# Performance work log

Measured on AMD Instinct MI355X. Metric: run time of the kernel, lower is better.

Reference implementation:

```python
import jax, jax.numpy as jnp
import numpy as np

B, S, D_IN, D_OUT, H = 2, 2048, 1024, 1024, 16
HEAD = D_OUT // H

def setup_inputs() -> dict:
    key = jax.random.key(0)
    ks = jax.random.split(key, 5)
    scale = 0.02
    return {
        "x": jax.random.normal(ks[0], (B, S, D_IN), dtype=jnp.float32),
        "Wq": jax.random.normal(ks[1], (D_OUT, D_IN), dtype=jnp.float32) * scale,
        "Wk": jax.random.normal(ks[2], (D_OUT, D_IN), dtype=jnp.float32) * scale,
        "Wv": jax.random.normal(ks[3], (D_OUT, D_IN), dtype=jnp.float32) * scale,
        "Wo": jax.random.normal(ks[4], (D_OUT, D_OUT), dtype=jnp.float32) * scale,
        "bo": jnp.zeros((D_OUT,), dtype=jnp.float32),
    }

def reference(x, Wq, Wk, Wv, Wo, bo):
    b, n, _ = x.shape
    # linear projections (torch Linear: y = x @ W.T)
    q = (x @ Wq.T).reshape(b, n, H, HEAD).transpose(0, 2, 1, 3)  # [b,h,n,d]
    k = (x @ Wk.T).reshape(b, n, H, HEAD).transpose(0, 2, 1, 3)
    v = (x @ Wv.T).reshape(b, n, H, HEAD).transpose(0, 2, 1, 3)
    scores = jnp.einsum('bhqd,bhkd->bhqk', q, k)  # [b,h,n,n]
    causal = jnp.triu(jnp.ones((n, n), dtype=bool), k=1)
    scores = jnp.where(causal, -jnp.inf, scores)
    # NOTE: original scales by sqrt(d_out**0.5) == d_out**0.25 (faithful quirk)
    inv_scale = jnp.float32(1.0 / (D_OUT ** 0.25))
    attn = jax.nn.softmax(scores * inv_scale, axis=-1)
    ctx = jnp.einsum('bhqk,bhkd->bhqd', attn, v)  # [b,h,n,d]
    ctx = ctx.transpose(0, 2, 1, 3).reshape(b, n, D_OUT)
    return ctx @ Wo.T + bo
```

## Files before the change

### kernel.cpp

```cpp
#include <hip/hip_runtime.h>

#define NB 2
#define NH 16
#define SEQ 2048
#define DM 1024
#define HD 64
#define MT (NB * SEQ)

typedef __attribute__((ext_vector_type(8))) short bf16x8;
typedef __attribute__((ext_vector_type(4))) float f32x4;

__device__ __forceinline__ unsigned short f2bf(float f) {
  union { float f; unsigned u; } v; v.f = f;
  return (unsigned short)((v.u + 0x7fffu + ((v.u >> 16) & 1u)) >> 16);
}

__device__ __forceinline__ void gld_lds16(const unsigned short* g, unsigned short* l) {
  __builtin_amdgcn_global_load_lds((const __attribute__((address_space(1))) unsigned int*)g,
                                   (__attribute__((address_space(3))) unsigned int*)l, 16, 0, 0);
}

__global__ __launch_bounds__(256) void cvt_all(const float* __restrict__ x,
                                               const float* __restrict__ wq,
                                               const float* __restrict__ wk,
                                               const float* __restrict__ wv,
                                               const float* __restrict__ wo,
                                               unsigned short* __restrict__ dst) {
  const int XQ = (MT * DM) / 4;
  const int WQ = (DM * DM) / 4;
  int i = blockIdx.x * 256 + threadIdx.x;
  const float* src; int base;
  if (i < XQ)               { src = x;  base = 0; }
  else if (i < XQ + WQ)     { src = wq; base = XQ; }
  else if (i < XQ + 2 * WQ) { src = wk; base = XQ + WQ; }
  else if (i < XQ + 3 * WQ) { src = wv; base = XQ + 2 * WQ; }
  else                      { src = wo; base = XQ + 3 * WQ; }
  float4 f = ((const float4*)src)[i - base];
  ushort4 u;
  u.x = f2bf(f.x); u.y = f2bf(f.y); u.z = f2bf(f.z); u.w = f2bf(f.w);
  ((ushort4*)dst)[i] = u;
}

#define LDT 32

__device__ __forceinline__ void gemm_bt_mainloop(const unsigned short* __restrict__ A,
                                                 const unsigned short* __restrict__ B,
                                                 int K,
                                                 unsigned short* As, unsigned short* Bs,
                                                 f32x4 acc[4][4]) {
  int tid = threadIdx.x;
  int lane = tid & 63, l15 = lane & 15, quad = lane >> 4;
  int w = tid >> 6, wm = (w >> 1) * 64, wn = (w & 1) * 64;
  int c0 = tid, c1 = tid + 256;
  int r0 = c0 >> 2, cc0 = (c0 & 3) * 8;
  int r1 = c1 >> 2, cc1 = (c1 & 3) * 8;
  const unsigned short* a0 = A + (size_t)r0 * K + cc0;
  const unsigned short* a1 = A + (size_t)r1 * K + cc1;
  const unsigned short* b0 = B + (size_t)r0 * K + cc0;
  const unsigned short* b1 = B + (size_t)r1 * K + cc1;
  unsigned short* la0 = As + c0 * 8;
  unsigned short* la1 = As + c1 * 8;
  unsigned short* lb0 = Bs + c0 * 8;
  unsigned short* lb1 = Bs + c1 * 8;

  for (int k0 = 0; k0 < K; k0 += 32) {
    gld_lds16(a0 + k0, la0);
    gld_lds16(a1 + k0, la1);
    gld_lds16(b0 + k0, lb0);
    gld_lds16(b1 + k0, lb1);
    __syncthreads();
    bf16x8 a[4], b[4];
#pragma unroll
    for (int i = 0; i < 4; ++i)
      a[i] = *(const bf16x8*)(As + (wm + i * 16 + l15) * LDT + 8 * quad);
#pragma unroll
    for (int i = 0; i < 4; ++i)
      b[i] = *(const bf16x8*)(Bs + (wn + i * 16 + l15) * LDT + 8 * quad);
#pragma unroll
    for (int i = 0; i < 4; ++i)
#pragma unroll
      for (int jj = 0; jj < 4; ++jj)
        acc[i][jj] = __builtin_amdgcn_mfma_f32_16x16x32_bf16(a[i], b[jj], acc[i][jj], 0, 0, 0);
    __syncthreads();
  }
}

#define QSCALE 0.2550565444f

__global__ __launch_bounds__(256) void gemm_qkv(const unsigned short* __restrict__ xb,
                                                const unsigned short* __restrict__ wcat,
                                                unsigned short* __restrict__ qb,
                                                unsigned short* __restrict__ kb,
                                                unsigned short* __restrict__ vtb) {
  __shared__ unsigned short As[128 * LDT], Bs[128 * LDT];
  int m0 = blockIdx.y * 128, n0 = blockIdx.x * 128;
  f32x4 acc[4][4];
#pragma unroll
  for (int i = 0; i < 4; ++i)
#pragma unroll
    for (int j = 0; j < 4; ++j) acc[i][j] = (f32x4){0.f, 0.f, 0.f, 0.f};

  gemm_bt_mainloop(xb + (size_t)m0 * DM, wcat + (size_t)n0 * DM, DM, As, Bs, acc);

  int tid = threadIdx.x, lane = tid & 63, l15 = lane & 15, quad = lane >> 4;
  int w = tid >> 6, wm = (w >> 1) * 64, wn = (w & 1) * 64;
  int mat = n0 >> 10;
#pragma unroll
  for (int i = 0; i < 4; ++i) {
    int mbase = m0 + wm + i * 16 + quad * 4;
    int bi = mbase >> 11, s = mbase & 2047;
#pragma unroll
    for (int j = 0; j < 4; ++j) {
      int n = n0 + wn + j * 16 + l15;
      int c = n & 1023, h = c >> 6, d = c & 63;
      if (mat == 2) {
        ushort4 u;
        u.x = f2bf(acc[i][j][0]); u.y = f2bf(acc[i][j][1]);
        u.z = f2bf(acc[i][j][2]); u.w = f2bf(acc[i][j][3]);
        *(ushort4*)(vtb + ((size_t)((bi * NH + h) * HD + d)) * SEQ + s) = u;
      } else {
        unsigned short* dst = (mat == 0) ? qb : kb;
        float sc = (mat == 0) ? QSCALE : 1.0f;
#pragma unroll
        for (int reg = 0; reg < 4; ++reg)
          dst[((size_t)((bi * NH + h) * SEQ + (s + reg))) * HD + d] = f2bf(acc[i][j][reg] * sc);
      }
    }
  }
}

#define LDQ 72

__global__ __launch_bounds__(512, 4) void attn_kernel(const unsigned short* __restrict__ qb,
                                                      const unsigned short* __restrict__ kb,
                                                      const unsigned short* __restrict__ vtb,
                                                      unsigned short* __restrict__ ctx) {
  __shared__ unsigned short QPs[128 * LDQ];
  __shared__ unsigned short Ks[64 * LDQ], Vts[64 * LDQ];
  int bx = blockIdx.x, h = blockIdx.y, bi = blockIdx.z;
  int qst = bi ? (15 - bx) : bx;
  int q0 = qst * 128;
  int tid = threadIdx.x, lane = tid & 63, l15 = lane & 15, quad = lane >> 4, w = tid >> 6;

  const unsigned short* qbase = qb + ((size_t)(bi * NH + h) * SEQ + q0) * HD;
  const unsigned short* kbase = kb + ((size_t)(bi * NH + h) * SEQ) * HD;
  const unsigned short* vbase = vtb + ((size_t)(bi * NH + h) * HD) * SEQ;

  {
    int c = tid, r = c >> 3, cc = (c & 7) * 8;
    *(int4*)(QPs + r * LDQ + cc) = *(const int4*)(qbase + (size_t)r * HD + cc);
    c = tid + 512; r = c >> 3; cc = (c & 7) * 8;
    *(int4*)(QPs + r * LDQ + cc) = *(const int4*)(qbase + (size_t)r * HD + cc);
  }
  int sr = tid >> 3, sc = (tid & 7) * 8;
  const unsigned short* kS = kbase + (size_t)sr * HD + sc;
  const unsigned short* vS = vbase + (size_t)sr * SEQ + sc;
  int4 kreg = *(const int4*)kS;
  int4 vreg = *(const int4*)vS;
  unsigned short* Kdst = Ks + sr * LDQ + sc;
  unsigned short* Vdst = Vts + sr * LDQ + sc;
  __syncthreads();

  bf16x8 aq0 = *(const bf16x8*)(QPs + (w * 16 + l15) * LDQ + 8 * quad);
  bf16x8 aq1 = *(const bf16x8*)(QPs + (w * 16 + l15) * LDQ + 32 + 8 * quad);

  f32x4 Oacc[4];
#pragma unroll
  for (int i = 0; i < 4; ++i) Oacc[i] = (f32x4){0.f, 0.f, 0.f, 0.f};
  float l_i[4] = {0.f, 0.f, 0.f, 0.f};
  int q0w = q0 + w * 16;
  int nkv = 2 * qst + 2;

  for (int j = 0; j < nkv; ++j) {
    int kv0 = j * 64;
    __syncthreads();
    *(int4*)Kdst = kreg;
    *(int4*)Vdst = vreg;
    __syncthreads();
    if (j + 1 < nkv) {
      kreg = *(const int4*)(kS + (size_t)(j + 1) * 64 * HD);
      vreg = *(const int4*)(vS + (j + 1) * 64);
    }
    if (kv0 <= q0w + 15) {
      f32x4 sacc[4];
#pragma unroll
      for (int ns = 0; ns < 4; ++ns) {
        bf16x8 bk0 = *(const bf16x8*)(Ks + (ns * 16 + l15) * LDQ + 8 * quad);
        bf16x8 bk1 = *(const bf16x8*)(Ks + (ns * 16 + l15) * LDQ + 32 + 8 * quad);
        sacc[ns] = (f32x4){0.f, 0.f, 0.f, 0.f};
        sacc[ns] = __builtin_amdgcn_mfma_f32_16x16x32_bf16(aq0, bk0, sacc[ns], 0, 0, 0);
        sacc[ns] = __builtin_amdgcn_mfma_f32_16x16x32_bf16(aq1, bk1, sacc[ns], 0, 0, 0);
      }
      bool needmask = (kv0 + 63) > q0w;
      float rs[4] = {0.f, 0.f, 0.f, 0.f};
#pragma unroll
      for (int ns = 0; ns < 4; ++ns)
#pragma unroll
        for (int reg = 0; reg < 4; ++reg) {
          float xv = sacc[ns][reg];
          if (needmask) {
            int kvg = kv0 + ns * 16 + l15;
            int qg = q0w + quad * 4 + reg;
            if (kvg > qg) xv = -INFINITY;
          }
          float p = __builtin_amdgcn_exp2f(xv);
          rs[reg] += p;
          QPs[(w * 16 + quad * 4 + reg) * LDQ + ns * 16 + l15] = f2bf(p);
        }
#pragma unroll
      for (int off = 1; off < 16; off <<= 1)
#pragma unroll
        for (int reg = 0; reg < 4; ++reg)
          rs[reg] += __shfl_xor(rs[reg], off, 64);
#pragma unroll
      for (int reg = 0; reg < 4; ++reg) l_i[reg] += rs[reg];

      bf16x8 pa0 = *(const bf16x8*)(QPs + (w * 16 + l15) * LDQ + 8 * quad);
      bf16x8 pa1 = *(const bf16x8*)(QPs + (w * 16 + l15) * LDQ + 32 + 8 * quad);
#pragma unroll
      for (int nd = 0; nd < 4; ++nd) {
        bf16x8 bv0 = *(const bf16x8*)(Vts + (nd * 16 + l15) * LDQ + 8 * quad);
        bf16x8 bv1 = *(const bf16x8*)(Vts + (nd * 16 + l15) * LDQ + 32 + 8 * quad);
        Oacc[nd] = __builtin_amdgcn_mfma_f32_16x16x32_bf16(pa0, bv0, Oacc[nd], 0, 0, 0);
        Oacc[nd] = __builtin_amdgcn_mfma_f32_16x16x32_bf16(pa1, bv1, Oacc[nd], 0, 0, 0);
      }
    }
  }

  float rl[4];
#pragma unroll
  for (int reg = 0; reg < 4; ++reg) rl[reg] = 1.0f / l_i[reg];
#pragma unroll
  for (int nd = 0; nd < 4; ++nd)
#pragma unroll
    for (int reg = 0; reg < 4; ++reg) {
      int s = q0w + quad * 4 + reg;
      int col = h * HD + nd * 16 + l15;
      ctx[((size_t)(bi * SEQ + s)) * DM + col] = f2bf(Oacc[nd][reg] * rl[reg]);
    }
}

__global__ __launch_bounds__(256) void gemm_out(const unsigned short* __restrict__ ctx,
                                                const unsigned short* __restrict__ wob,
                                                const float* __restrict__ bo,
                                                float* __restrict__ out) {
  __shared__ unsigned short As[128 * LDT], Bs[128 * LDT];
  int m0 = blockIdx.y * 128, n0 = blockIdx.x * 128;
  f32x4 acc[4][4];
#pragma unroll
  for (int i = 0; i < 4; ++i)
#pragma unroll
    for (int j = 0; j < 4; ++j) acc[i][j] = (f32x4){0.f, 0.f, 0.f, 0.f};

  gemm_bt_mainloop(ctx + (size_t)m0 * DM, wob + (size_t)n0 * DM, DM, As, Bs, acc);

  int tid = threadIdx.x, lane = tid & 63, l15 = lane & 15, quad = lane >> 4;
  int w = tid >> 6, wm = (w >> 1) * 64, wn = (w & 1) * 64;
#pragma unroll
  for (int i = 0; i < 4; ++i)
#pragma unroll
    for (int j = 0; j < 4; ++j) {
      int n = n0 + wn + j * 16 + l15;
      float bias = bo[n];
#pragma unroll
      for (int reg = 0; reg < 4; ++reg) {
        int m = m0 + wm + i * 16 + quad * 4 + reg;
        out[(size_t)m * DM + n] = acc[i][j][reg] + bias;
      }
    }
}

extern "C" void kernel_launch(void* const* d_in, const int* in_sizes, int n_in,
                              void* d_out, int out_size, void* d_ws, size_t ws_size,
                              hipStream_t stream) {
  const float* x  = (const float*)d_in[0];
  const float* Wq = (const float*)d_in[1];
  const float* Wk = (const float*)d_in[2];
  const float* Wv = (const float*)d_in[3];
  const float* Wo = (const float*)d_in[4];
  const float* bo = (const float*)d_in[5];
  float* out = (float*)d_out;

  unsigned short* ws = (unsigned short*)d_ws;
  unsigned short* xb   = ws;
  unsigned short* ctx  = ws;
  unsigned short* wcat = ws + (size_t)MT * DM;
  unsigned short* wob  = wcat + (size_t)3 * DM * DM;
  unsigned short* qb   = wob + (size_t)DM * DM;
  unsigned short* kb   = qb + (size_t)MT * DM;
  unsigned short* vtb  = kb + (size_t)MT * DM;

  int totalq = (MT * DM + 4 * DM * DM) / 4;
  cvt_all<<<totalq / 256, 256, 0, stream>>>(x, Wq, Wk, Wv, Wo, ws);

  gemm_qkv<<<dim3(24, 32), 256, 0, stream>>>(xb, wcat, qb, kb, vtb);
  attn_kernel<<<dim3(16, NH, NB), 512, 0, stream>>>(qb, kb, vtb, ctx);
  gemm_out<<<dim3(8, 32), 256, 0, stream>>>(ctx, wob, bo, out);
}
```

Measured before the change: 208.4 us.

## Widen GEMM K-tile with XOR-swizzled LDS and use 128-wide KV tiles in attention

The shared GEMM mainloop now stages 64-wide K slices with an XOR swizzle on the LDS layout, which halves the number of barrier pairs and is meant to avoid bank conflicts. Both GEMMs also get a launch-bounds occupancy hint. The attention kernel processes 128-key tiles per iteration and skips score MFMAs past the causal diagonal on the last tile, zero-filling the leftover P columns. It also converts P to bf16 by truncation instead of round-to-nearest, trading a small amount of precision for fewer ALU ops. LDS use and register pressure per block grow.

```diff
diff --git a/kernel.cpp b/kernel.cpp
--- a/kernel.cpp
+++ b/kernel.cpp
@@ -41,8 +41,6 @@
   ((ushort4*)dst)[i] = u;
 }
 
-#define LDT 32
-
 __device__ __forceinline__ void gemm_bt_mainloop(const unsigned short* __restrict__ A,
                                                  const unsigned short* __restrict__ B,
                                                  int K,
@@ -51,48 +49,55 @@
   int tid = threadIdx.x;
   int lane = tid & 63, l15 = lane & 15, quad = lane >> 4;
   int w = tid >> 6, wm = (w >> 1) * 64, wn = (w & 1) * 64;
-  int c0 = tid, c1 = tid + 256;
-  int r0 = c0 >> 2, cc0 = (c0 & 3) * 8;
-  int r1 = c1 >> 2, cc1 = (c1 & 3) * 8;
-  const unsigned short* a0 = A + (size_t)r0 * K + cc0;
-  const unsigned short* a1 = A + (size_t)r1 * K + cc1;
-  const unsigned short* b0 = B + (size_t)r0 * K + cc0;
-  const unsigned short* b1 = B + (size_t)r1 * K + cc1;
-  unsigned short* la0 = As + c0 * 8;
-  unsigned short* la1 = As + c1 * 8;
-  unsigned short* lb0 = Bs + c0 * 8;
-  unsigned short* lb1 = Bs + c1 * 8;
-
-  for (int k0 = 0; k0 < K; k0 += 32) {
-    gld_lds16(a0 + k0, la0);
-    gld_lds16(a1 + k0, la1);
-    gld_lds16(b0 + k0, lb0);
-    gld_lds16(b1 + k0, lb1);
+  int gofs[4];
+#pragma unroll
+  for (int it = 0; it < 4; ++it) {
+    int c = tid + it * 256;
+    int r = c >> 3, pos = c & 7;
+    gofs[it] = r * K + ((pos ^ (r & 7)) * 8);
+  }
+  for (int k0 = 0; k0 < K; k0 += 64) {
+#pragma unroll
+    for (int it = 0; it < 4; ++it)
+      gld_lds16(A + k0 + gofs[it], As + (tid + it * 256) * 8);
+#pragma unroll
+    for (int it = 0; it < 4; ++it)
+      gld_lds16(B + k0 + gofs[it], Bs + (tid + it * 256) * 8);
     __syncthreads();
-    bf16x8 a[4], b[4];
-#pragma unroll
-    for (int i = 0; i < 4; ++i)
-      a[i] = *(const bf16x8*)(As + (wm + i * 16 + l15) * LDT + 8 * quad);
-#pragma unroll
-    for (int i = 0; i < 4; ++i)
-      b[i] = *(const bf16x8*)(Bs + (wn + i * 16 + l15) * LDT + 8 * quad);
-#pragma unroll
-    for (int i = 0; i < 4; ++i)
-#pragma unroll
-      for (int jj = 0; jj < 4; ++jj)
-        acc[i][jj] = __builtin_amdgcn_mfma_f32_16x16x32_bf16(a[i], b[jj], acc[i][jj], 0, 0, 0);
+    bf16x8 a[4][2], b[4][2];
+#pragma unroll
+    for (int i = 0; i < 4; ++i) {
+      int row = wm + i * 16 + l15, sw = row & 7;
+#pragma unroll
+      for (int s = 0; s < 2; ++s)
+        a[i][s] = *(const bf16x8*)(As + row * 64 + (((quad + 4 * s) ^ sw) * 8));
+    }
+#pragma unroll
+    for (int i = 0; i < 4; ++i) {
+      int row = wn + i * 16 + l15, sw = row & 7;
+#pragma unroll
+      for (int s = 0; s < 2; ++s)
+        b[i][s] = *(const bf16x8*)(Bs + row * 64 + (((quad + 4 * s) ^ sw) * 8));
+    }
+#pragma unroll
+    for (int s = 0; s < 2; ++s)
+#pragma unroll
+      for (int i = 0; i < 4; ++i)
+#pragma unroll
+        for (int jj = 0; jj < 4; ++jj)
+          acc[i][jj] = __builtin_amdgcn_mfma_f32_16x16x32_bf16(a[i][s], b[jj][s], acc[i][jj], 0, 0, 0);
     __syncthreads();
   }
 }
 
 #define QSCALE 0.2550565444f
 
-__global__ __launch_bounds__(256) void gemm_qkv(const unsigned short* __restrict__ xb,
-                                                const unsigned short* __restrict__ wcat,
-                                                unsigned short* __restrict__ qb,
-                                                unsigned short* __restrict__ kb,
-                                                unsigned short* __restrict__ vtb) {
-  __shared__ unsigned short As[128 * LDT], Bs[128 * LDT];
+__global__ __launch_bounds__(256, 3) void gemm_qkv(const unsigned short* __restrict__ xb,
+                                                   const unsigned short* __restrict__ wcat,
+                                                   unsigned short* __restrict__ qb,
+                                                   unsigned short* __restrict__ kb,
+                                                   unsigned short* __restrict__ vtb) {
+  __shared__ unsigned short As[128 * 64], Bs[128 * 64];
   int m0 = blockIdx.y * 128, n0 = blockIdx.x * 128;
   f32x4 acc[4][4];
 #pragma unroll
@@ -129,14 +134,17 @@
   }
 }
 
-#define LDQ 72
+#define LP 136
+#define LDK 72
+#define LV 136
 
 __global__ __launch_bounds__(512, 4) void attn_kernel(const unsigned short* __restrict__ qb,
                                                       const unsigned short* __restrict__ kb,
                                                       const unsigned short* __restrict__ vtb,
                                                       unsigned short* __restrict__ ctx) {
-  __shared__ unsigned short QPs[128 * LDQ];
-  __shared__ unsigned short Ks[64 * LDQ], Vts[64 * LDQ];
+  __shared__ unsigned short Ps[128 * LP];
+  __shared__ unsigned short Ks[128 * LDK];
+  __shared__ unsigned short Vts[64 * LV];
   int bx = blockIdx.x, h = blockIdx.y, bi = blockIdx.z;
   int qst = bi ? (15 - bx) : bx;
   int q0 = qst * 128;
@@ -148,81 +156,99 @@
 
   {
     int c = tid, r = c >> 3, cc = (c & 7) * 8;
-    *(int4*)(QPs + r * LDQ + cc) = *(const int4*)(qbase + (size_t)r * HD + cc);
+    *(int4*)(Ps + r * LP + cc) = *(const int4*)(qbase + (size_t)r * HD + cc);
     c = tid + 512; r = c >> 3; cc = (c & 7) * 8;
-    *(int4*)(QPs + r * LDQ + cc) = *(const int4*)(qbase + (size_t)r * HD + cc);
-  }
-  int sr = tid >> 3, sc = (tid & 7) * 8;
-  const unsigned short* kS = kbase + (size_t)sr * HD + sc;
-  const unsigned short* vS = vbase + (size_t)sr * SEQ + sc;
-  int4 kreg = *(const int4*)kS;
-  int4 vreg = *(const int4*)vS;
-  unsigned short* Kdst = Ks + sr * LDQ + sc;
-  unsigned short* Vdst = Vts + sr * LDQ + sc;
+    *(int4*)(Ps + r * LP + cc) = *(const int4*)(qbase + (size_t)r * HD + cc);
+  }
+  int kr = tid >> 3, kc = (tid & 7) * 8;
+  int vr = tid >> 4, vc = (tid & 15) * 8;
+  const unsigned short* kS0 = kbase + (size_t)kr * HD + kc;
+  const unsigned short* kS1 = kS0 + (size_t)64 * HD;
+  const unsigned short* vS0 = vbase + (size_t)vr * SEQ + vc;
+  const unsigned short* vS1 = vS0 + (size_t)32 * SEQ;
+  int4 kreg0 = *(const int4*)kS0, kreg1 = *(const int4*)kS1;
+  int4 vreg0 = *(const int4*)vS0, vreg1 = *(const int4*)vS1;
+  unsigned short* Kd0 = Ks + kr * LDK + kc;
+  unsigned short* Kd1 = Kd0 + 64 * LDK;
+  unsigned short* Vd0 = Vts + vr * LV + vc;
+  unsigned short* Vd1 = Vd0 + 32 * LV;
   __syncthreads();
 
-  bf16x8 aq0 = *(const bf16x8*)(QPs + (w * 16 + l15) * LDQ + 8 * quad);
-  bf16x8 aq1 = *(const bf16x8*)(QPs + (w * 16 + l15) * LDQ + 32 + 8 * quad);
+  bf16x8 aq0 = *(const bf16x8*)(Ps + (w * 16 + l15) * LP + 8 * quad);
+  bf16x8 aq1 = *(const bf16x8*)(Ps + (w * 16 + l15) * LP + 32 + 8 * quad);
 
   f32x4 Oacc[4];
 #pragma unroll
   for (int i = 0; i < 4; ++i) Oacc[i] = (f32x4){0.f, 0.f, 0.f, 0.f};
   float l_i[4] = {0.f, 0.f, 0.f, 0.f};
   int q0w = q0 + w * 16;
-  int nkv = 2 * qst + 2;
-
-  for (int j = 0; j < nkv; ++j) {
-    int kv0 = j * 64;
+  int nt = qst + 1;
+
+  for (int j = 0; j < nt; ++j) {
+    int kv0 = j * 128;
     __syncthreads();
-    *(int4*)Kdst = kreg;
-    *(int4*)Vdst = vreg;
+    *(int4*)Kd0 = kreg0; *(int4*)Kd1 = kreg1;
+    *(int4*)Vd0 = vreg0; *(int4*)Vd1 = vreg1;
     __syncthreads();
-    if (j + 1 < nkv) {
-      kreg = *(const int4*)(kS + (size_t)(j + 1) * 64 * HD);
-      vreg = *(const int4*)(vS + (j + 1) * 64);
-    }
-    if (kv0 <= q0w + 15) {
-      f32x4 sacc[4];
-#pragma unroll
-      for (int ns = 0; ns < 4; ++ns) {
-        bf16x8 bk0 = *(const bf16x8*)(Ks + (ns * 16 + l15) * LDQ + 8 * quad);
-        bf16x8 bk1 = *(const bf16x8*)(Ks + (ns * 16 + l15) * LDQ + 32 + 8 * quad);
-        sacc[ns] = (f32x4){0.f, 0.f, 0.f, 0.f};
-        sacc[ns] = __builtin_amdgcn_mfma_f32_16x16x32_bf16(aq0, bk0, sacc[ns], 0, 0, 0);
-        sacc[ns] = __builtin_amdgcn_mfma_f32_16x16x32_bf16(aq1, bk1, sacc[ns], 0, 0, 0);
-      }
-      bool needmask = (kv0 + 63) > q0w;
-      float rs[4] = {0.f, 0.f, 0.f, 0.f};
-#pragma unroll
-      for (int ns = 0; ns < 4; ++ns)
-#pragma unroll
-        for (int reg = 0; reg < 4; ++reg) {
-          float xv = sacc[ns][reg];
-          if (needmask) {
-            int kvg = kv0 + ns * 16 + l15;
-            int qg = q0w + quad * 4 + reg;
-            if (kvg > qg) xv = -INFINITY;
-          }
-          float p = __builtin_amdgcn_exp2f(xv);
-          rs[reg] += p;
-          QPs[(w * 16 + quad * 4 + reg) * LDQ + ns * 16 + l15] = f2bf(p);
+    if (j + 1 < nt) {
+      size_t ko = (size_t)(j + 1) * 128 * HD;
+      int vo = (j + 1) * 128;
+      kreg0 = *(const int4*)(kS0 + ko); kreg1 = *(const int4*)(kS1 + ko);
+      vreg0 = *(const int4*)(vS0 + vo); vreg1 = *(const int4*)(vS1 + vo);
+    }
+    bool diag = (j == nt - 1);
+    int ns_hi = diag ? ((q0w + 15 - kv0) >> 4) : 7;
+    int s_hi = ns_hi >> 1;
+
+    float rs[4] = {0.f, 0.f, 0.f, 0.f};
+#pragma unroll
+    for (int ns = 0; ns < 8; ++ns) {
+      if (ns > ns_hi) break;
+      bf16x8 bk0 = *(const bf16x8*)(Ks + (ns * 16 + l15) * LDK + 8 * quad);
+      bf16x8 bk1 = *(const bf16x8*)(Ks + (ns * 16 + l15) * LDK + 32 + 8 * quad);
+      f32x4 s = (f32x4){0.f, 0.f, 0.f, 0.f};
+      s = __builtin_amdgcn_mfma_f32_16x16x32_bf16(aq0, bk0, s, 0, 0, 0);
+      s = __builtin_amdgcn_mfma_f32_16x16x32_bf16(aq1, bk1, s, 0, 0, 0);
+      bool m = diag && (ns == ns_hi);
+#pragma unroll
+      for (int reg = 0; reg < 4; ++reg) {
+        float xv = s[reg];
+        if (m) {
+          int kvg = kv0 + ns * 16 + l15;
+          int qg = q0w + quad * 4 + reg;
+          if (kvg > qg) xv = -INFINITY;
         }
-#pragma unroll
-      for (int off = 1; off < 16; off <<= 1)
+        float p = __builtin_amdgcn_exp2f(xv);
+        rs[reg] += p;
+        union { float f; unsigned u; } pu; pu.f = p;
+        Ps[(w * 16 + quad * 4 + reg) * LP + ns * 16 + l15] = (unsigned short)(pu.u >> 16);
+      }
+    }
+    if (diag) {
+#pragma unroll
+      for (int ns = 0; ns < 8; ++ns) {
+        if (ns <= ns_hi || ns > 2 * s_hi + 1) continue;
 #pragma unroll
         for (int reg = 0; reg < 4; ++reg)
-          rs[reg] += __shfl_xor(rs[reg], off, 64);
-#pragma unroll
-      for (int reg = 0; reg < 4; ++reg) l_i[reg] += rs[reg];
-
-      bf16x8 pa0 = *(const bf16x8*)(QPs + (w * 16 + l15) * LDQ + 8 * quad);
-      bf16x8 pa1 = *(const bf16x8*)(QPs + (w * 16 + l15) * LDQ + 32 + 8 * quad);
+          Ps[(w * 16 + quad * 4 + reg) * LP + ns * 16 + l15] = 0;
+      }
+    }
+#pragma unroll
+    for (int off = 1; off < 16; off <<= 1)
+#pragma unroll
+      for (int reg = 0; reg < 4; ++reg)
+        rs[reg] += __shfl_xor(rs[reg], off, 64);
+#pragma unroll
+    for (int reg = 0; reg < 4; ++reg) l_i[reg] += rs[reg];
+
+#pragma unroll
+    for (int step = 0; step < 4; ++step) {
+      if (step > s_hi) break;
+      bf16x8 pa = *(const bf16x8*)(Ps + (w * 16 + l15) * LP + 8 * quad + 32 * step);
 #pragma unroll
       for (int nd = 0; nd < 4; ++nd) {
-        bf16x8 bv0 = *(const bf16x8*)(Vts + (nd * 16 + l15) * LDQ + 8 * quad);
-        bf16x8 bv1 = *(const bf16x8*)(Vts + (nd * 16 + l15) * LDQ + 32 + 8 * quad);
-        Oacc[nd] = __builtin_amdgcn_mfma_f32_16x16x32_bf16(pa0, bv0, Oacc[nd], 0, 0, 0);
-        Oacc[nd] = __builtin_amdgcn_mfma_f32_16x16x32_bf16(pa1, bv1, Oacc[nd], 0, 0, 0);
+        bf16x8 bv = *(const bf16x8*)(Vts + (nd * 16 + l15) * LV + 8 * quad + 32 * step);
+        Oacc[nd] = __builtin_amdgcn_mfma_f32_16x16x32_bf16(pa, bv, Oacc[nd], 0, 0, 0);
       }
     }
   }
@@ -240,11 +266,11 @@
     }
 }
 
-__global__ __launch_bounds__(256) void gemm_out(const unsigned short* __restrict__ ctx,
-                                                const unsigned short* __restrict__ wob,
-                                                const float* __restrict__ bo,
-                                                float* __restrict__ out) {
-  __shared__ unsigned short As[128 * LDT], Bs[128 * LDT];
+__global__ __launch_bounds__(256, 3) void gemm_out(const unsigned short* __restrict__ ctx,
+                                                   const unsigned short* __restrict__ wob,
+                                                   const float* __restrict__ bo,
+                                                   float* __restrict__ out) {
+  __shared__ unsigned short As[128 * 64], Bs[128 * 64];
   int m0 = blockIdx.y * 128, n0 = blockIdx.x * 128;
   f32x4 acc[4][4];
 #pragma unroll
```

Result: faster. 176.1 us (-15.5%).
